# Optimization experiments

Hardware: AMD Instinct MI355X
Metric: run time of the kernel (lower is better)

Reference implementation:

```python
import jax, jax.numpy as jnp
import numpy as np

B, P, J, MOT, K, NB, WN, H = 64, 12273, 80, 94, 64, 20, 17, 128
W_POSE = 1.0

def euler_to_rotmat(a):
    # a: [..., 3] radians, R = Rz @ Ry @ Rx
    sx, sy, sz = jnp.sin(a[..., 0]), jnp.sin(a[..., 1]), jnp.sin(a[..., 2])
    cx, cy, cz = jnp.cos(a[..., 0]), jnp.cos(a[..., 1]), jnp.cos(a[..., 2])
    r00 = cz * cy; r01 = cz * sy * sx - sz * cx; r02 = cz * sy * cx + sz * sx
    r10 = sz * cy; r11 = sz * sy * sx + cz * cx; r12 = sz * sy * cx - cz * sx
    r20 = -sy;     r21 = cy * sx;                r22 = cy * cx
    return jnp.stack([jnp.stack([r00, r01, r02], -1),
                      jnp.stack([r10, r11, r12], -1),
                      jnp.stack([r20, r21, r22], -1)], -2)

def setup_inputs() -> dict:
    key = jax.random.key(0)
    ks = jax.random.split(key, 20)
    f32 = jnp.float32
    return {
        'in_pc_batch': jax.random.normal(ks[0], (B, P, 3), f32),
        't_nor': jax.random.normal(ks[1], (B, P, 3), f32),
        'rest_verts': jax.random.normal(ks[2], (P, 3), f32),
        'skin_weights': jax.random.uniform(ks[3], (P, J), f32),
        'mul_weight_list': jax.random.normal(ks[4], (J, MOT), f32),
        'query': jax.random.normal(ks[5], (B, J, 3), f32),
        'cloth_pose_std': jax.random.uniform(ks[6], (3,), f32),
        'cloth_pose_mean': jax.random.normal(ks[7], (3,), f32),
        'cloth_trans_std': jax.random.uniform(ks[8], (3,), f32),
        'cloth_trans_mean': jax.random.normal(ks[9], (3,), f32),
        'W1': jax.random.normal(ks[10], (3 + K, H), f32) * 0.1,
        'b1': jnp.zeros((H,), f32),
        'W2': jax.random.normal(ks[11], (H, 6), f32) * 0.1,
        'b2': jnp.zeros((6,), f32),
        'tmtemp': jax.random.normal(ks[12], (B, MOT, K), f32),
        'Wd': jax.random.normal(ks[13], (MOT * K, NB * WN), f32) * 0.02,
        'bd': jnp.zeros((NB * WN,), f32),
        'DPSD': jax.random.normal(ks[14], (NB, WN, P, 3), f32) * 0.1,
        'ssdr_res_std': jax.random.uniform(ks[15], (3,), f32),
        'ssdr_res_mean': jax.random.normal(ks[16], (3,), f32),
    }

def reference(in_pc_batch, t_nor, rest_verts, skin_weights, mul_weight_list,
              query, cloth_pose_std, cloth_pose_mean, cloth_trans_std,
              cloth_trans_mean, W1, b1, W2, b2, tmtemp, Wd, bd, DPSD,
              ssdr_res_std, ssdr_res_mean):
    # per-joint field input: [B, J, K]
    field_input = jnp.einsum('bjk,lj->blk', tmtemp, jax.nn.relu(mul_weight_list))
    # FieldNet: per-joint MLP on concat(query, field_input) -> [B, J, 6]
    h = jnp.concatenate([query, field_input], axis=-1)
    pred_rt = jax.nn.relu(h @ W1 + b1) @ W2 + b2
    pred_pose = pred_rt[..., 0:3] * cloth_pose_std + cloth_pose_mean
    pred_trans = (query + pred_rt[..., 3:6]) * cloth_trans_std + cloth_trans_mean
    # detailsnet + fused 20-basis accumulation: [B, P, 3]
    nbat = tmtemp.shape[0]
    detailkey = (tmtemp.reshape(nbat, -1) @ Wd + bd).reshape(nbat, NB, WN)
    detail_res = jnp.einsum('bnw,nwpx->bpx', detailkey, DPSD)
    detail_res = detail_res * ssdr_res_std + ssdr_res_mean
    # SSDR LBS skinning with Euler-angle rotations (degrees -> radians)
    R = euler_to_rotmat(jnp.deg2rad(pred_pose))            # [B, J, 3, 3]
    skinned = (jnp.einsum('pj,bjxy,py->bpx', skin_weights, R, rest_verts)
               + jnp.einsum('pj,bjx->bpx', skin_weights, pred_trans))
    out_pc = skinned + detail_res                          # [B, P, 3]
    loss_pose_l1 = jnp.mean(jnp.abs(in_pc_batch[:, :, 0:3] - out_pc))
    loss = loss_pose_l1 * W_POSE + 1e-4 * jnp.mean(DPSD ** 2)
    return loss[None], out_pc
```

## Files before the change

kernel.cpp:

```cpp
#include <hip/hip_runtime.h>

#define B_   64
#define P_   12273
#define J_   80
#define MOT_ 94
#define K_   64
#define H_   128
#define Q_   340
#define NE_  36819
#define MK_  6016
#define PW_  12288

typedef float v4f  __attribute__((ext_vector_type(4)));
typedef float v8f  __attribute__((ext_vector_type(8)));
typedef float v16f __attribute__((ext_vector_type(16)));
#define AS4 __attribute__((address_space(4)))

__device__ __forceinline__ const AS4 float* unif(const float* p){
  return (const AS4 float*)(unsigned long long)p;
}
__device__ __forceinline__ const AS4 v4f* univ4(const float* p){
  return (const AS4 v4f*)(unsigned long long)p;
}
__device__ __forceinline__ const AS4 v8f* univ8(const float* p){
  return (const AS4 v8f*)(unsigned long long)p;
}
__device__ __forceinline__ const AS4 v16f* univ16(const float* p){
  return (const AS4 v16f*)(unsigned long long)p;
}

__global__ __launch_bounds__(256) void k_prep(
    const float* __restrict__ query, const float* __restrict__ mwl,
    const float* __restrict__ tm,    const float* __restrict__ W1,
    const float* __restrict__ b1,    const float* __restrict__ W2,
    const float* __restrict__ b2,    const float* __restrict__ cps,
    const float* __restrict__ cpm,   const float* __restrict__ cts,
    const float* __restrict__ ctm,   const float* __restrict__ skin,
    float* __restrict__ G,           float* __restrict__ tm_t,
    float* __restrict__ w_t,         float* __restrict__ lacc)
{
  __shared__ float smem[80 * 65];
  int blk = blockIdx.x;
  int t = threadIdx.x;
  if (blk < 1280){
    int lane = t & 63;
    int wid = __builtin_amdgcn_readfirstlane(t >> 6);
    int bj = blk * 4 + wid;
    int b = bj / J_, l = bj - b * J_;
    float* hs = smem + wid * 80;
    float acc = 0.f;
    const AS4 float* mp = unif(mwl + l * MOT_);
    const float* tp = tm + (size_t)b * MK_ + lane;
    #pragma unroll 2
    for (int j = 0; j < MOT_; j++){
      float w = mp[j]; w = w > 0.f ? w : 0.f;
      acc = fmaf(w, tp[j * K_], acc);
    }
    hs[3 + lane] = acc;
    if (lane < 3) hs[lane] = query[(size_t)bj * 3 + lane];
    __syncthreads();
    float a1 = b1[lane], a2 = b1[lane + 64];
    for (int i = 0; i < 3 + K_; i++){
      float hv = hs[i];
      a1 = fmaf(hv, W1[i * H_ + lane], a1);
      a2 = fmaf(hv, W1[i * H_ + 64 + lane], a2);
    }
    a1 = a1 > 0.f ? a1 : 0.f;
    a2 = a2 > 0.f ? a2 : 0.f;
    const AS4 float* b2c = unif(b2);
    float rt[6];
    #pragma unroll
    for (int o = 0; o < 6; o++){
      float po = fmaf(a1, W2[lane * 6 + o], a2 * W2[(lane + 64) * 6 + o]);
      #pragma unroll
      for (int off = 32; off; off >>= 1) po += __shfl_xor(po, off);
      rt[o] = po + b2c[o];
    }
    const float D2R = 0.017453292519943295f;
    float ax = fmaf(rt[0], cps[0], cpm[0]) * D2R;
    float ay = fmaf(rt[1], cps[1], cpm[1]) * D2R;
    float az = fmaf(rt[2], cps[2], cpm[2]) * D2R;
    float tx = fmaf(hs[0] + rt[3], cts[0], ctm[0]);
    float ty = fmaf(hs[1] + rt[4], cts[1], ctm[1]);
    float tz = fmaf(hs[2] + rt[5], cts[2], ctm[2]);
    float sx, cx, sy, cy, sz, cz;
    sincosf(ax, &sx, &cx); sincosf(ay, &sy, &cy); sincosf(az, &sz, &cz);
    if (lane == 0){
      float4 r0 = make_float4(cz*cy, cz*sy*sx - sz*cx, cz*sy*cx + sz*sx, tx);
      float4 r1 = make_float4(sz*cy, sz*sy*sx + cz*cx, sz*sy*cx - cz*sx, ty);
      float4 r2 = make_float4(-sy,   cy*sx,            cy*cx,            tz);
      float4* g = (float4*)(G + (size_t)bj * 12);
      g[0] = r0; g[1] = r1; g[2] = r2;
    }
  } else if (blk < 1374){
    int m0 = (blk - 1280) * 64;
    int ml = t & 63, g = t >> 6;
    #pragma unroll
    for (int r = 0; r < 16; r++){
      int b = g * 16 + r;
      smem[ml * 65 + b] = tm[(size_t)b * MK_ + m0 + ml];
    }
    __syncthreads();
    int bl = t & 63;
    #pragma unroll
    for (int r = 0; r < 16; r++){
      int m = g * 16 + r;
      tm_t[(size_t)(m0 + m) * 64 + bl] = smem[m * 65 + bl];
    }
  } else if (blk < 1566){
    int p0 = (blk - 1374) * 64;
    #pragma unroll
    for (int k = 0; k < 20; k++){
      int idx = k * 256 + t;
      int pl = idx / 80, j = idx - pl * 80;
      int p = p0 + pl;
      smem[j * 65 + pl] = (p < P_) ? skin[(size_t)p * J_ + j] : 0.f;
    }
    __syncthreads();
    #pragma unroll
    for (int k = 0; k < 20; k++){
      int idx = k * 256 + t;
      int j = idx >> 6, pl = idx & 63;
      w_t[(size_t)j * PW_ + p0 + pl] = smem[j * 65 + pl];
    }
  } else {
    if (t < 2) lacc[t] = 0.f;
  }
}

__global__ __launch_bounds__(256) void k_dkey(
    const float* __restrict__ tm_t, const float* __restrict__ Wd,
    float* __restrict__ part)
{
  int t = threadIdx.x;
  int lane = t & 63;
  int wid = __builtin_amdgcn_readfirstlane(t >> 6);
  int qt = blockIdx.x;
  int q = qt * 64 + lane;
  bool vq = q < Q_;
  int m0 = blockIdx.y * 64;
  const AS4 v16f* tr = univ16(tm_t);
  float acc[16];
  #pragma unroll
  for (int i = 0; i < 16; i++) acc[i] = 0.f;
  float wbuf[4];
  #pragma unroll
  for (int i = 0; i < 4; i++)
    wbuf[i] = vq ? Wd[(size_t)(m0 + i) * Q_ + q] : 0.f;
  v16f tb0 = tr[(size_t)(m0 + 0) * 4 + wid];
  v16f tb1 = tr[(size_t)(m0 + 1) * 4 + wid];
  #pragma unroll 4
  for (int mm = 0; mm < 60; mm++){
    float wd = wbuf[mm & 3];
    wbuf[mm & 3] = vq ? Wd[(size_t)(m0 + mm + 4) * Q_ + q] : 0.f;
    v16f tv = tb0; tb0 = tb1;
    tb1 = tr[(size_t)(m0 + mm + 2) * 4 + wid];
    #pragma unroll
    for (int i = 0; i < 16; i++) acc[i] = fmaf(tv[i], wd, acc[i]);
  }
  #pragma unroll
  for (int mm = 60; mm < 64; mm++){
    float wd = wbuf[mm & 3];
    v16f tv = tb0; tb0 = tb1;
    if (mm < 62) tb1 = tr[(size_t)(m0 + mm + 2) * 4 + wid];
    #pragma unroll
    for (int i = 0; i < 16; i++) acc[i] = fmaf(tv[i], wd, acc[i]);
  }
  float* pb = part + ((size_t)blockIdx.y * 6 + qt) * 4096 + (size_t)(wid * 16) * 64;
  #pragma unroll
  for (int i = 0; i < 16; i++) pb[i * 64 + lane] = acc[i];
}

__global__ __launch_bounds__(256) void k_dkred(
    const float* __restrict__ part, const float* __restrict__ bd,
    float* __restrict__ dk_t, int S)
{
  int t = threadIdx.x;
  int jj = blockIdx.x * 32 + (t >> 3);
  int dl = t & 7;
  int b = jj / Q_, q = jj - b * Q_;
  int qt = q >> 6, ql = q & 63;
  const float* pp = part + (size_t)qt * 4096 + b * 64 + ql;
  float s = 0.f;
  for (int d = dl; d < S; d += 8) s += pp[(size_t)d * 6 * 4096];
  s += __shfl_xor(s, 1); s += __shfl_xor(s, 2); s += __shfl_xor(s, 4);
  if (dl == 0) dk_t[q * 64 + b] = bd[q] + s;
}

__device__ __forceinline__ void dconsume(const AS4 v16f* dkv, int qa, int wid,
                                         const float* dc, float* acc,
                                         float& sq, bool doSq)
{
  v16f r0 = dkv[(qa + 0) * 4 + wid];
  v16f r1 = dkv[(qa + 1) * 4 + wid];
  v16f r2 = dkv[(qa + 2) * 4 + wid];
  v16f r3 = dkv[(qa + 3) * 4 + wid];
  v16f r4 = dkv[(qa + 4) * 4 + wid];
  if (doSq){
    #pragma unroll
    for (int i = 0; i < 5; i++) sq = fmaf(dc[i], dc[i], sq);
  }
  #pragma unroll
  for (int i = 0; i < 16; i++){
    acc[i] = fmaf(r0[i], dc[0], acc[i]);
    acc[i] = fmaf(r1[i], dc[1], acc[i]);
    acc[i] = fmaf(r2[i], dc[2], acc[i]);
    acc[i] = fmaf(r3[i], dc[3], acc[i]);
    acc[i] = fmaf(r4[i], dc[4], acc[i]);
  }
}

__global__ __launch_bounds__(256) void k_detail(
    const float* __restrict__ DPSD, const float* __restrict__ dk_t,
    float* __restrict__ stg0, float* __restrict__ out,
    float* __restrict__ lacc, int qn)
{
  int t = threadIdx.x;
  int lane = t & 63;
  int wid = __builtin_amdgcn_readfirstlane(t >> 6);
  int b0 = wid * 16;
  int e = blockIdx.x * 64 + lane;
  bool ve = e < NE_;
  int q0 = blockIdx.y * qn;
  const AS4 v16f* dkv = univ16(dk_t);
  const float* Dp = DPSD + (ve ? e : 0);
  float acc[16];
  #pragma unroll
  for (int i = 0; i < 16; i++) acc[i] = 0.f;
  float sq = 0.f;
  bool doSq = (wid == 0);
  float da[5], db[5];
  #pragma unroll
  for (int i = 0; i < 5; i++) da[i] = Dp[(size_t)(q0 + i) * NE_];
  #pragma unroll
  for (int i = 0; i < 5; i++) db[i] = Dp[(size_t)(q0 + 5 + i) * NE_];
  int ng = qn / 5;
  int g = 0;
  for (; g + 2 < ng; g += 2){
    int qa = q0 + g * 5;
    float ta[5], tb[5];
    #pragma unroll
    for (int i = 0; i < 5; i++) ta[i] = Dp[(size_t)(qa + 10 + i) * NE_];
    dconsume(dkv, qa, wid, da, acc, sq, doSq);
    #pragma unroll
    for (int i = 0; i < 5; i++) da[i] = ta[i];
    #pragma unroll
    for (int i = 0; i < 5; i++) tb[i] = Dp[(size_t)(qa + 15 + i) * NE_];
    dconsume(dkv, qa + 5, wid, db, acc, sq, doSq);
    #pragma unroll
    for (int i = 0; i < 5; i++) db[i] = tb[i];
  }
  dconsume(dkv, q0 + (ng - 2) * 5, wid, da, acc, sq, doSq);
  dconsume(dkv, q0 + (ng - 1) * 5, wid, db, acc, sq, doSq);
  if (ve){
    bool toOut = (blockIdx.y + 1 == gridDim.y);
    float* dst = toOut ? (out + 1 + e) : (stg0 + e);
    #pragma unroll
    for (int i = 0; i < 16; i++)
      dst[(size_t)(b0 + i) * NE_] = acc[i];
  }
  if (doSq){
    if (!ve) sq = 0.f;
    #pragma unroll
    for (int off = 32; off; off >>= 1) sq += __shfl_xor(sq, off);
    if (lane == 0) atomicAdd(&lacc[1], sq);
  }
}

__global__ __launch_bounds__(256) void k_skin(
    const float* __restrict__ G, const float* __restrict__ w_t,
    const float* __restrict__ rest, const float* __restrict__ in_pc,
    const float* __restrict__ stg0, const float* __restrict__ rstd,
    const float* __restrict__ rmean,
    float* __restrict__ out, float* __restrict__ lacc, int two)
{
  int t = threadIdx.x;
  int lane = t & 63;
  int wid = __builtin_amdgcn_readfirstlane(t >> 6);
  int p  = blockIdx.x * 64 + lane;
  int bA = blockIdx.y * 8 + wid * 2;
  const AS4 v4f* gA = univ4(G + (size_t)bA * J_ * 12);
  const AS4 v4f* gB = univ4(G + ((size_t)bA + 1) * J_ * 12);
  float accA[12], accB[12];
  #pragma unroll
  for (int c = 0; c < 12; c++){ accA[c] = 0.f; accB[c] = 0.f; }
  const float* wp = w_t + p;
  #pragma unroll 4
  for (int j = 0; j < J_; j++){
    float w = wp[(size_t)j * PW_];
    v4f a0 = gA[j * 3 + 0], a1 = gA[j * 3 + 1], a2 = gA[j * 3 + 2];
    v4f c0 = gB[j * 3 + 0], c1 = gB[j * 3 + 1], c2 = gB[j * 3 + 2];
    #pragma unroll
    for (int c = 0; c < 4; c++){
      accA[c]     = fmaf(w, a0[c], accA[c]);
      accA[4 + c] = fmaf(w, a1[c], accA[4 + c]);
      accA[8 + c] = fmaf(w, a2[c], accA[8 + c]);
      accB[c]     = fmaf(w, c0[c], accB[c]);
      accB[4 + c] = fmaf(w, c1[c], accB[4 + c]);
      accB[8 + c] = fmaf(w, c2[c], accB[8 + c]);
    }
  }
  bool vp = p < P_;
  float vx = 0.f, vy = 0.f, vz = 0.f;
  if (vp){ vx = rest[p * 3]; vy = rest[p * 3 + 1]; vz = rest[p * 3 + 2]; }
  float srs[3], srm[3];
  #pragma unroll
  for (int x = 0; x < 3; x++){ srs[x] = rstd[x]; srm[x] = rmean[x]; }
  float lsum = 0.f;
  if (vp){
    size_t baseA = ((size_t)bA * P_ + p) * 3;
    size_t baseB = baseA + (size_t)P_ * 3;
    #pragma unroll
    for (int x = 0; x < 3; x++){
      float det = out[1 + baseA + x];
      if (two) det += stg0[baseA + x];
      float v = fmaf(accA[x*4+0], vx, fmaf(accA[x*4+1], vy, fmaf(accA[x*4+2], vz, accA[x*4+3])));
      v += fmaf(det, srs[x], srm[x]);
      lsum += fabsf(in_pc[baseA + x] - v);
      out[1 + baseA + x] = v;
    }
    #pragma unroll
    for (int x = 0; x < 3; x++){
      float det = out[1 + baseB + x];
      if (two) det += stg0[baseB + x];
      float v = fmaf(accB[x*4+0], vx, fmaf(accB[x*4+1], vy, fmaf(accB[x*4+2], vz, accB[x*4+3])));
      v += fmaf(det, srs[x], srm[x]);
      lsum += fabsf(in_pc[baseB + x] - v);
      out[1 + baseB + x] = v;
    }
  }
  #pragma unroll
  for (int off = 32; off; off >>= 1) lsum += __shfl_xor(lsum, off);
  __shared__ float red[4];
  if (lane == 0) red[wid] = lsum;
  __syncthreads();
  if (t == 0) atomicAdd(&lacc[0], red[0] + red[1] + red[2] + red[3]);
}

__global__ void k_finalize(const float* __restrict__ lacc, float* __restrict__ out){
  if (threadIdx.x == 0 && blockIdx.x == 0){
    float loss = lacc[0] * (1.f / 2356416.f) + 1e-4f * (lacc[1] * (1.f / 12518460.f));
    out[0] = loss;
  }
}

extern "C" void kernel_launch(void* const* d_in, const int* in_sizes, int n_in,
                              void* d_out, int out_size, void* d_ws, size_t ws_size,
                              hipStream_t stream){
  const float* in_pc = (const float*)d_in[0];
  const float* rest  = (const float*)d_in[2];
  const float* skin  = (const float*)d_in[3];
  const float* mwl   = (const float*)d_in[4];
  const float* query = (const float*)d_in[5];
  const float* cps   = (const float*)d_in[6];
  const float* cpm   = (const float*)d_in[7];
  const float* cts   = (const float*)d_in[8];
  const float* ctm   = (const float*)d_in[9];
  const float* W1    = (const float*)d_in[10];
  const float* b1    = (const float*)d_in[11];
  const float* W2    = (const float*)d_in[12];
  const float* b2    = (const float*)d_in[13];
  const float* tm    = (const float*)d_in[14];
  const float* Wd    = (const float*)d_in[15];
  const float* bd    = (const float*)d_in[16];
  const float* DPSD  = (const float*)d_in[17];
  const float* rstd  = (const float*)d_in[18];
  const float* rmean = (const float*)d_in[19];
  float* out = (float*)d_out;

  float* ws   = (float*)d_ws;
  float* G    = ws;
  float* dk_t = G + 61440;
  float* lacc = dk_t + 21760;
  float* tm_t = lacc + 64;
  float* w_t  = tm_t + 385024;
  float* un   = w_t + 983040;

  size_t have = ws_size / 4;
  int nqh = (have >= (size_t)(1451328 + 2356416)) ? 2 : 1;
  int qn = Q_ / nqh;

  k_prep    <<<1567, 256, 0, stream>>>(query, mwl, tm, W1, b1, W2, b2,
                                       cps, cpm, cts, ctm, skin,
                                       G, tm_t, w_t, lacc);
  k_dkey    <<<dim3(6, 94), 256, 0, stream>>>(tm_t, Wd, un);
  k_dkred   <<<680, 256, 0, stream>>>(un, bd, dk_t, 94);
  k_detail  <<<dim3(576, nqh), 256, 0, stream>>>(DPSD, dk_t, un, out, lacc, qn);
  k_skin    <<<dim3(192, 8), 256, 0, stream>>>(G, w_t, rest, in_pc, un, rstd, rmean,
                                               out, lacc, nqh - 1);
  k_finalize<<<1, 64, 0, stream>>>(lacc, out);
}
```

Before: 255.5 us.

## Replace dkey reduction kernel with atomics, deepen prefetch, split detail 4-way, stage G in LDS

Removes the separate k_dkred kernel: dk_t is initialised with the bias in k_prep and k_dkey accumulates its partial sums directly into dk_t with atomicAdd. Register prefetch depth is increased in k_prep, k_dkey, k_detail and k_skin to hide global load latency. k_detail can now split the 340 basis terms four ways when workspace allows, and k_skin sums the extra staging buffers. k_skin also copies its G block into shared memory. Together these aim to cut a launch, expose more parallelism in the DPSD stream and reduce load stalls. The cost is atomic contention, non-deterministic summation order, and extra staging traffic.

```diff
diff --git a/kernel.cpp b/kernel.cpp
--- a/kernel.cpp
+++ b/kernel.cpp
@@ -10,6 +10,7 @@
 #define NE_  36819
 #define MK_  6016
 #define PW_  12288
+#define STG_ 2356416
 
 typedef float v4f  __attribute__((ext_vector_type(4)));
 typedef float v8f  __attribute__((ext_vector_type(8)));
@@ -21,9 +22,6 @@
 }
 __device__ __forceinline__ const AS4 v4f* univ4(const float* p){
   return (const AS4 v4f*)(unsigned long long)p;
-}
-__device__ __forceinline__ const AS4 v8f* univ8(const float* p){
-  return (const AS4 v8f*)(unsigned long long)p;
 }
 __device__ __forceinline__ const AS4 v16f* univ16(const float* p){
   return (const AS4 v16f*)(unsigned long long)p;
@@ -36,8 +34,10 @@
     const float* __restrict__ b2,    const float* __restrict__ cps,
     const float* __restrict__ cpm,   const float* __restrict__ cts,
     const float* __restrict__ ctm,   const float* __restrict__ skin,
+    const float* __restrict__ bd,
     float* __restrict__ G,           float* __restrict__ tm_t,
-    float* __restrict__ w_t,         float* __restrict__ lacc)
+    float* __restrict__ w_t,         float* __restrict__ dk_t,
+    float* __restrict__ lacc)
 {
   __shared__ float smem[80 * 65];
   int blk = blockIdx.x;
@@ -51,19 +51,36 @@
     float acc = 0.f;
     const AS4 float* mp = unif(mwl + l * MOT_);
     const float* tp = tm + (size_t)b * MK_ + lane;
-    #pragma unroll 2
+    float tbuf[4];
+    #pragma unroll
+    for (int s = 0; s < 4; s++) tbuf[s] = tp[s * K_];
+    #pragma unroll 4
     for (int j = 0; j < MOT_; j++){
+      float tv = tbuf[j & 3];
+      if (j + 4 < MOT_) tbuf[j & 3] = tp[(j + 4) * K_];
       float w = mp[j]; w = w > 0.f ? w : 0.f;
-      acc = fmaf(w, tp[j * K_], acc);
+      acc = fmaf(w, tv, acc);
     }
     hs[3 + lane] = acc;
     if (lane < 3) hs[lane] = query[(size_t)bj * 3 + lane];
     __syncthreads();
     float a1 = b1[lane], a2 = b1[lane + 64];
-    for (int i = 0; i < 3 + K_; i++){
+    float wa[4], wb[4];
+    #pragma unroll
+    for (int s = 0; s < 4; s++){
+      wa[s] = W1[s * H_ + lane];
+      wb[s] = W1[s * H_ + 64 + lane];
+    }
+    #pragma unroll 4
+    for (int i = 0; i < 67; i++){
       float hv = hs[i];
-      a1 = fmaf(hv, W1[i * H_ + lane], a1);
-      a2 = fmaf(hv, W1[i * H_ + 64 + lane], a2);
+      float va = wa[i & 3], vb = wb[i & 3];
+      if (i + 4 < 67){
+        wa[i & 3] = W1[(i + 4) * H_ + lane];
+        wb[i & 3] = W1[(i + 4) * H_ + 64 + lane];
+      }
+      a1 = fmaf(hv, va, a1);
+      a2 = fmaf(hv, vb, a2);
     }
     a1 = a1 > 0.f ? a1 : 0.f;
     a2 = a2 > 0.f ? a2 : 0.f;
@@ -123,6 +140,9 @@
       int j = idx >> 6, pl = idx & 63;
       w_t[(size_t)j * PW_ + p0 + pl] = smem[j * 65 + pl];
     }
+  } else if (blk < 1651){
+    int idx = (blk - 1566) * 256 + t;
+    dk_t[idx] = bd[idx >> 6];
   } else {
     if (t < 2) lacc[t] = 0.f;
   }
@@ -130,7 +150,7 @@
 
 __global__ __launch_bounds__(256) void k_dkey(
     const float* __restrict__ tm_t, const float* __restrict__ Wd,
-    float* __restrict__ part)
+    float* __restrict__ dk_t)
 {
   int t = threadIdx.x;
   int lane = t & 63;
@@ -143,53 +163,32 @@
   float acc[16];
   #pragma unroll
   for (int i = 0; i < 16; i++) acc[i] = 0.f;
-  float wbuf[4];
-  #pragma unroll
-  for (int i = 0; i < 4; i++)
-    wbuf[i] = vq ? Wd[(size_t)(m0 + i) * Q_ + q] : 0.f;
-  v16f tb0 = tr[(size_t)(m0 + 0) * 4 + wid];
-  v16f tb1 = tr[(size_t)(m0 + 1) * 4 + wid];
-  #pragma unroll 4
-  for (int mm = 0; mm < 60; mm++){
-    float wd = wbuf[mm & 3];
-    wbuf[mm & 3] = vq ? Wd[(size_t)(m0 + mm + 4) * Q_ + q] : 0.f;
-    v16f tv = tb0; tb0 = tb1;
-    tb1 = tr[(size_t)(m0 + mm + 2) * 4 + wid];
+  float wbuf[8];
+  #pragma unroll
+  for (int s = 0; s < 8; s++)
+    wbuf[s] = vq ? Wd[(size_t)(m0 + s) * Q_ + q] : 0.f;
+  v16f tb[4];
+  #pragma unroll
+  for (int s = 0; s < 4; s++) tb[s] = tr[(size_t)(m0 + s) * 4 + wid];
+  #pragma unroll 8
+  for (int mm = 0; mm < 64; mm++){
+    float wd = wbuf[mm & 7];
+    if (mm + 8 < 64) wbuf[mm & 7] = vq ? Wd[(size_t)(m0 + mm + 8) * Q_ + q] : 0.f;
+    v16f tv = tb[mm & 3];
+    if (mm + 4 < 64) tb[mm & 3] = tr[(size_t)(m0 + mm + 4) * 4 + wid];
     #pragma unroll
     for (int i = 0; i < 16; i++) acc[i] = fmaf(tv[i], wd, acc[i]);
   }
-  #pragma unroll
-  for (int mm = 60; mm < 64; mm++){
-    float wd = wbuf[mm & 3];
-    v16f tv = tb0; tb0 = tb1;
-    if (mm < 62) tb1 = tr[(size_t)(m0 + mm + 2) * 4 + wid];
-    #pragma unroll
-    for (int i = 0; i < 16; i++) acc[i] = fmaf(tv[i], wd, acc[i]);
-  }
-  float* pb = part + ((size_t)blockIdx.y * 6 + qt) * 4096 + (size_t)(wid * 16) * 64;
-  #pragma unroll
-  for (int i = 0; i < 16; i++) pb[i * 64 + lane] = acc[i];
-}
-
-__global__ __launch_bounds__(256) void k_dkred(
-    const float* __restrict__ part, const float* __restrict__ bd,
-    float* __restrict__ dk_t, int S)
-{
-  int t = threadIdx.x;
-  int jj = blockIdx.x * 32 + (t >> 3);
-  int dl = t & 7;
-  int b = jj / Q_, q = jj - b * Q_;
-  int qt = q >> 6, ql = q & 63;
-  const float* pp = part + (size_t)qt * 4096 + b * 64 + ql;
-  float s = 0.f;
-  for (int d = dl; d < S; d += 8) s += pp[(size_t)d * 6 * 4096];
-  s += __shfl_xor(s, 1); s += __shfl_xor(s, 2); s += __shfl_xor(s, 4);
-  if (dl == 0) dk_t[q * 64 + b] = bd[q] + s;
-}
-
-__device__ __forceinline__ void dconsume(const AS4 v16f* dkv, int qa, int wid,
-                                         const float* dc, float* acc,
-                                         float& sq, bool doSq)
+  if (vq){
+    float* dp = dk_t + (size_t)q * 64 + wid * 16;
+    #pragma unroll
+    for (int i = 0; i < 16; i++) atomicAdd(&dp[i], acc[i]);
+  }
+}
+
+__device__ __forceinline__ void dk_consume(const AS4 v16f* dkv, int qa, int wid,
+                                           const float* dc, float* acc,
+                                           float& sq, bool doSq)
 {
   v16f r0 = dkv[(qa + 0) * 4 + wid];
   v16f r1 = dkv[(qa + 1) * 4 + wid];
@@ -212,7 +211,7 @@
 
 __global__ __launch_bounds__(256) void k_detail(
     const float* __restrict__ DPSD, const float* __restrict__ dk_t,
-    float* __restrict__ stg0, float* __restrict__ out,
+    float* __restrict__ stg, float* __restrict__ out,
     float* __restrict__ lacc, int qn)
 {
   int t = threadIdx.x;
@@ -229,32 +228,32 @@
   for (int i = 0; i < 16; i++) acc[i] = 0.f;
   float sq = 0.f;
   bool doSq = (wid == 0);
-  float da[5], db[5];
-  #pragma unroll
-  for (int i = 0; i < 5; i++) da[i] = Dp[(size_t)(q0 + i) * NE_];
-  #pragma unroll
-  for (int i = 0; i < 5; i++) db[i] = Dp[(size_t)(q0 + 5 + i) * NE_];
   int ng = qn / 5;
-  int g = 0;
-  for (; g + 2 < ng; g += 2){
-    int qa = q0 + g * 5;
-    float ta[5], tb[5];
-    #pragma unroll
-    for (int i = 0; i < 5; i++) ta[i] = Dp[(size_t)(qa + 10 + i) * NE_];
-    dconsume(dkv, qa, wid, da, acc, sq, doSq);
-    #pragma unroll
-    for (int i = 0; i < 5; i++) da[i] = ta[i];
-    #pragma unroll
-    for (int i = 0; i < 5; i++) tb[i] = Dp[(size_t)(qa + 15 + i) * NE_];
-    dconsume(dkv, qa + 5, wid, db, acc, sq, doSq);
-    #pragma unroll
-    for (int i = 0; i < 5; i++) db[i] = tb[i];
-  }
-  dconsume(dkv, q0 + (ng - 2) * 5, wid, da, acc, sq, doSq);
-  dconsume(dkv, q0 + (ng - 1) * 5, wid, db, acc, sq, doSq);
+  float buf[4][5];
+  #pragma unroll
+  for (int s = 0; s < 4; s++){
+    #pragma unroll
+    for (int i = 0; i < 5; i++)
+      buf[s][i] = Dp[(size_t)(q0 + s * 5 + i) * NE_];
+  }
+  for (int g = 0; g < ng; g += 4){
+    #pragma unroll
+    for (int s = 0; s < 4; s++){
+      int gg = g + s;
+      if (gg < ng){
+        dk_consume(dkv, q0 + gg * 5, wid, buf[s], acc, sq, doSq);
+        int gp = gg + 4;
+        if (gp < ng){
+          #pragma unroll
+          for (int i = 0; i < 5; i++)
+            buf[s][i] = Dp[(size_t)(q0 + gp * 5 + i) * NE_];
+        }
+      }
+    }
+  }
   if (ve){
     bool toOut = (blockIdx.y + 1 == gridDim.y);
-    float* dst = toOut ? (out + 1 + e) : (stg0 + e);
+    float* dst = toOut ? (out + 1 + e) : (stg + (size_t)blockIdx.y * STG_ + e);
     #pragma unroll
     for (int i = 0; i < 16; i++)
       dst[(size_t)(b0 + i) * NE_] = acc[i];
@@ -270,35 +269,54 @@
 __global__ __launch_bounds__(256) void k_skin(
     const float* __restrict__ G, const float* __restrict__ w_t,
     const float* __restrict__ rest, const float* __restrict__ in_pc,
-    const float* __restrict__ stg0, const float* __restrict__ rstd,
+    const float* __restrict__ stg, const float* __restrict__ rstd,
     const float* __restrict__ rmean,
-    float* __restrict__ out, float* __restrict__ lacc, int two)
+    float* __restrict__ out, float* __restrict__ lacc, int nst)
 {
+  __shared__ float gs[7680];
+  __shared__ float red[4];
   int t = threadIdx.x;
   int lane = t & 63;
   int wid = __builtin_amdgcn_readfirstlane(t >> 6);
+  {
+    const float4* Gv = (const float4*)(G + (size_t)blockIdx.y * 7680);
+    float4* gv = (float4*)gs;
+    #pragma unroll
+    for (int it = 0; it < 8; it++){
+      int idx = it * 256 + t;
+      if (idx < 1920) gv[idx] = Gv[idx];
+    }
+  }
+  __syncthreads();
   int p  = blockIdx.x * 64 + lane;
   int bA = blockIdx.y * 8 + wid * 2;
-  const AS4 v4f* gA = univ4(G + (size_t)bA * J_ * 12);
-  const AS4 v4f* gB = univ4(G + ((size_t)bA + 1) * J_ * 12);
+  const float4* gsA = (const float4*)(gs + (wid * 2) * 960);
+  const float4* gsB = gsA + 240;
   float accA[12], accB[12];
   #pragma unroll
   for (int c = 0; c < 12; c++){ accA[c] = 0.f; accB[c] = 0.f; }
   const float* wp = w_t + p;
-  #pragma unroll 4
+  float wbuf[8];
+  #pragma unroll
+  for (int s = 0; s < 8; s++) wbuf[s] = wp[(size_t)s * PW_];
+  #pragma unroll 8
   for (int j = 0; j < J_; j++){
-    float w = wp[(size_t)j * PW_];
-    v4f a0 = gA[j * 3 + 0], a1 = gA[j * 3 + 1], a2 = gA[j * 3 + 2];
-    v4f c0 = gB[j * 3 + 0], c1 = gB[j * 3 + 1], c2 = gB[j * 3 + 2];
-    #pragma unroll
-    for (int c = 0; c < 4; c++){
-      accA[c]     = fmaf(w, a0[c], accA[c]);
-      accA[4 + c] = fmaf(w, a1[c], accA[4 + c]);
-      accA[8 + c] = fmaf(w, a2[c], accA[8 + c]);
-      accB[c]     = fmaf(w, c0[c], accB[c]);
-      accB[4 + c] = fmaf(w, c1[c], accB[4 + c]);
-      accB[8 + c] = fmaf(w, c2[c], accB[8 + c]);
-    }
+    float w = wbuf[j & 7];
+    if (j + 8 < J_) wbuf[j & 7] = wp[(size_t)(j + 8) * PW_];
+    float4 a0 = gsA[j * 3], a1 = gsA[j * 3 + 1], a2 = gsA[j * 3 + 2];
+    float4 c0 = gsB[j * 3], c1 = gsB[j * 3 + 1], c2 = gsB[j * 3 + 2];
+    accA[0]  = fmaf(w, a0.x, accA[0]);  accA[1]  = fmaf(w, a0.y, accA[1]);
+    accA[2]  = fmaf(w, a0.z, accA[2]);  accA[3]  = fmaf(w, a0.w, accA[3]);
+    accA[4]  = fmaf(w, a1.x, accA[4]);  accA[5]  = fmaf(w, a1.y, accA[5]);
+    accA[6]  = fmaf(w, a1.z, accA[6]);  accA[7]  = fmaf(w, a1.w, accA[7]);
+    accA[8]  = fmaf(w, a2.x, accA[8]);  accA[9]  = fmaf(w, a2.y, accA[9]);
+    accA[10] = fmaf(w, a2.z, accA[10]); accA[11] = fmaf(w, a2.w, accA[11]);
+    accB[0]  = fmaf(w, c0.x, accB[0]);  accB[1]  = fmaf(w, c0.y, accB[1]);
+    accB[2]  = fmaf(w, c0.z, accB[2]);  accB[3]  = fmaf(w, c0.w, accB[3]);
+    accB[4]  = fmaf(w, c1.x, accB[4]);  accB[5]  = fmaf(w, c1.y, accB[5]);
+    accB[6]  = fmaf(w, c1.z, accB[6]);  accB[7]  = fmaf(w, c1.w, accB[7]);
+    accB[8]  = fmaf(w, c2.x, accB[8]);  accB[9]  = fmaf(w, c2.y, accB[9]);
+    accB[10] = fmaf(w, c2.z, accB[10]); accB[11] = fmaf(w, c2.w, accB[11]);
   }
   bool vp = p < P_;
   float vx = 0.f, vy = 0.f, vz = 0.f;
@@ -313,7 +331,7 @@
     #pragma unroll
     for (int x = 0; x < 3; x++){
       float det = out[1 + baseA + x];
-      if (two) det += stg0[baseA + x];
+      for (int s = 0; s < nst; s++) det += stg[(size_t)s * STG_ + baseA + x];
       float v = fmaf(accA[x*4+0], vx, fmaf(accA[x*4+1], vy, fmaf(accA[x*4+2], vz, accA[x*4+3])));
       v += fmaf(det, srs[x], srm[x]);
       lsum += fabsf(in_pc[baseA + x] - v);
@@ -322,7 +340,7 @@
     #pragma unroll
     for (int x = 0; x < 3; x++){
       float det = out[1 + baseB + x];
-      if (two) det += stg0[baseB + x];
+      for (int s = 0; s < nst; s++) det += stg[(size_t)s * STG_ + baseB + x];
       float v = fmaf(accB[x*4+0], vx, fmaf(accB[x*4+1], vy, fmaf(accB[x*4+2], vz, accB[x*4+3])));
       v += fmaf(det, srs[x], srm[x]);
       lsum += fabsf(in_pc[baseB + x] - v);
@@ -331,7 +349,6 @@
   }
   #pragma unroll
   for (int off = 32; off; off >>= 1) lsum += __shfl_xor(lsum, off);
-  __shared__ float red[4];
   if (lane == 0) red[wid] = lsum;
   __syncthreads();
   if (t == 0) atomicAdd(&lacc[0], red[0] + red[1] + red[2] + red[3]);
@@ -374,19 +391,21 @@
   float* lacc = dk_t + 21760;
   float* tm_t = lacc + 64;
   float* w_t  = tm_t + 385024;
-  float* un   = w_t + 983040;
+  float* stg  = w_t + 983040;
 
   size_t have = ws_size / 4;
-  int nqh = (have >= (size_t)(1451328 + 2356416)) ? 2 : 1;
+  const size_t base = 1451328;
+  int nqh = 1;
+  if (have >= base + 3 * (size_t)STG_)      nqh = 4;
+  else if (have >= base + (size_t)STG_)     nqh = 2;
   int qn = Q_ / nqh;
 
-  k_prep    <<<1567, 256, 0, stream>>>(query, mwl, tm, W1, b1, W2, b2,
-                                       cps, cpm, cts, ctm, skin,
-                                       G, tm_t, w_t, lacc);
-  k_dkey    <<<dim3(6, 94), 256, 0, stream>>>(tm_t, Wd, un);
-  k_dkred   <<<680, 256, 0, stream>>>(un, bd, dk_t, 94);
-  k_detail  <<<dim3(576, nqh), 256, 0, stream>>>(DPSD, dk_t, un, out, lacc, qn);
-  k_skin    <<<dim3(192, 8), 256, 0, stream>>>(G, w_t, rest, in_pc, un, rstd, rmean,
+  k_prep    <<<1652, 256, 0, stream>>>(query, mwl, tm, W1, b1, W2, b2,
+                                       cps, cpm, cts, ctm, skin, bd,
+                                       G, tm_t, w_t, dk_t, lacc);
+  k_dkey    <<<dim3(6, 94), 256, 0, stream>>>(tm_t, Wd, dk_t);
+  k_detail  <<<dim3(576, nqh), 256, 0, stream>>>(DPSD, dk_t, stg, out, lacc, qn);
+  k_skin    <<<dim3(192, 8), 256, 0, stream>>>(G, w_t, rest, in_pc, stg, rstd, rmean,
                                                out, lacc, nqh - 1);
   k_finalize<<<1, 64, 0, stream>>>(lacc, out);
 }
```

New measurement: 453.1 us. +77.4%, slower.
